# Kernel tuning notes

Hardware: AMD Instinct MI355X
Metric: run time of the kernel (lower is better)

## Reference

```python
import jax, jax.numpy as jnp
import numpy as np

DEPTH = 256
HEADS = 8
K = 128          # kernel_size == attended axis length (height)
DH = DEPTH // HEADS  # 32
EPS = 1e-5


def _bn(x, gamma, beta, axes):
    # training-mode batch norm (biased variance), per-channel on axis 1
    mean = jnp.mean(x, axis=axes, keepdims=True)
    var = jnp.var(x, axis=axes, keepdims=True)
    shape = [1] * x.ndim
    shape[1] = x.shape[1]
    g = gamma.reshape(shape)
    b = beta.reshape(shape)
    return (x - mean) * jax.lax.rsqrt(var + EPS) * g + b


def setup_inputs() -> dict:
    key = jax.random.key(0)
    ks = jax.random.split(key, 3)
    x = jax.random.normal(ks[0], (2, DEPTH, K, K), dtype=jnp.float32)
    w_kqv = jax.random.normal(ks[1], (2 * DEPTH, DEPTH), dtype=jnp.float32) * 0.05
    rel_encoding = jax.random.normal(ks[2], (2 * DH, 2 * K - 1), dtype=jnp.float32)
    return {
        "x": x,
        "w_kqv": w_kqv,
        "kqv_gamma": jnp.ones((2 * DEPTH,), jnp.float32),
        "kqv_beta": jnp.zeros((2 * DEPTH,), jnp.float32),
        "logits_gamma": jnp.ones((3 * HEADS,), jnp.float32),
        "logits_beta": jnp.zeros((3 * HEADS,), jnp.float32),
        "rel_encoding": rel_encoding,
    }


def reference(x, w_kqv, kqv_gamma, kqv_beta, logits_gamma, logits_beta, rel_encoding):
    B, C, H, W = x.shape  # height_dim=True path
    # (B,C,H,W) -> (B,W,C,H) -> (B*W, C, H)
    xf = jnp.transpose(x, (0, 3, 1, 2)).reshape(B * W, C, H)
    # 1x1 conv == channel matmul
    kqv = jnp.einsum('oc,bch->boh', w_kqv, xf)  # (BW, 2*depth, H)
    kqv = _bn(kqv, kqv_gamma, kqv_beta, axes=(0, 2))
    kqv = kqv.reshape(B * W, HEADS, 2 * DH, H)
    k = kqv[:, :, : DH // 2]            # (BW, h, dh/2, H)
    q = kqv[:, :, DH // 2: DH]          # (BW, h, dh/2, H)
    v = kqv[:, :, DH:]                  # (BW, h, dh,   H)

    # relative position gather: (2*dh, 2K-1) -> (2*dh, K, K)
    idx = (jnp.arange(K)[None, :] - jnp.arange(K)[:, None] + K - 1).reshape(-1)
    rel = rel_encoding[:, idx].reshape(2 * DH, K, K)
    q_enc = rel[: DH // 2]
    k_enc = rel[DH // 2: DH]
    v_enc = rel[DH:]

    qk = jnp.einsum('bhdx,bhdy->bhxy', q, k)
    qr = jnp.einsum('bhdx,dxy->bhxy', q, q_enc)
    kr = jnp.swapaxes(jnp.einsum('bhdx,dxy->bhxy', k, k_enc), 2, 3)
    logits = jnp.concatenate([qk, qr, kr], axis=1)  # (BW, 3*h, K, K)
    logits = _bn(logits, logits_gamma, logits_beta, axes=(0, 2, 3))
    logits = logits.reshape(B * W, 3, HEADS, H, H).sum(axis=1)
    weights = jax.nn.softmax(logits, axis=3)  # (BW, h, K, K)

    attn = jnp.einsum('bhxy,bhdy->bhdx', weights, v)         # (BW, h, dh, H)
    attn_enc = jnp.einsum('bhxy,dxy->bhdx', weights, v_enc)  # (BW, h, dh, H)
    out = (attn + attn_enc).reshape(B, W, DEPTH, H)  # cat+reshape+sum(dim=-2) == add
    out = jnp.transpose(out, (0, 2, 3, 1))  # (B, depth, H, W)
    return out
```

## Files before the change

kernel.cpp:

```cpp
#include <hip/hip_runtime.h>
#include <hip/hip_bf16.h>

#define H 128
#define NB 256
#define OC 512
#define CIN 256
#define NN 16384
#define EPS 1e-5f

typedef __attribute__((ext_vector_type(4))) float f32x4;
typedef __attribute__((ext_vector_type(8))) short bf16x8;
typedef unsigned short u16x8 __attribute__((ext_vector_type(8)));

__device__ __forceinline__ float bf2f(unsigned short u){
    return __uint_as_float(((unsigned int)u) << 16);
}
__device__ __forceinline__ unsigned short f2bf(float f){
    unsigned int x = __float_as_uint(f);
    return (unsigned short)((x + 0x7fffu + ((x >> 16) & 1u)) >> 16);
}
__device__ __forceinline__ float ldin(const void* p, size_t i, bool f32){
    return f32 ? ((const float*)p)[i] : bf2f(((const unsigned short*)p)[i]);
}
__device__ __forceinline__ short ld_bf16(const void* p, size_t i, bool f32){
    if (f32) return (short)f2bf(((const float*)p)[i]);
    return ((const short*)p)[i];
}
__device__ __forceinline__ bool probe_f32(const void* gamma_ones){
    return *(const unsigned int*)gamma_ones == 0x3F800000u;
}

template<bool F32>
__device__ __forceinline__ void gemm_body(const void* __restrict__ w,
                                          const void* __restrict__ x,
                                          unsigned short* __restrict__ c1,
                                          short (*As)[128][40], short (*Bs)[64][40])
{
    const int m0 = blockIdx.x * 128;
    const int n0 = blockIdx.y * 64;
    const int b0 = blockIdx.z;
    const int t  = threadIdx.x;
    const int lane = t & 63, wv = t >> 6;
    const int wm = wv & 1, wn = wv >> 1;
    const int lm = lane & 15, quad = lane >> 4;
    const size_t xb = (size_t)b0 * CIN * NN;
    const int am = t >> 1, ak = (t & 1) * 16;
    const int bn = t & 63, bk = (t >> 6) * 8;

    float4 pa[4]; float pb[8];
    u16x8 qa[2]; unsigned short qb[8];

    auto load_tile = [&](int k0){
        if constexpr (F32){
            const float* wp = (const float*)w + (size_t)(m0+am)*CIN + k0 + ak;
            #pragma unroll
            for (int q=0;q<4;q++) pa[q] = *(const float4*)(wp + 4*q);
            const float* xp = (const float*)x + xb + (size_t)(k0+bk)*NN + n0 + bn;
            #pragma unroll
            for (int i=0;i<8;i++) pb[i] = xp[(size_t)i*NN];
        } else {
            const unsigned short* wp = (const unsigned short*)w + (size_t)(m0+am)*CIN + k0 + ak;
            qa[0] = *(const u16x8*)wp; qa[1] = *(const u16x8*)(wp+8);
            const unsigned short* xp = (const unsigned short*)x + xb + (size_t)(k0+bk)*NN + n0 + bn;
            #pragma unroll
            for (int i=0;i<8;i++) qb[i] = xp[(size_t)i*NN];
        }
    };
    auto store_tile = [&](int buf){
        if constexpr (F32){
            short ta[16];
            #pragma unroll
            for (int q=0;q<4;q++){
                ta[4*q+0]=(short)f2bf(pa[q].x); ta[4*q+1]=(short)f2bf(pa[q].y);
                ta[4*q+2]=(short)f2bf(pa[q].z); ta[4*q+3]=(short)f2bf(pa[q].w);
            }
            *(bf16x8*)&As[buf][am][ak]   = *(bf16x8*)&ta[0];
            *(bf16x8*)&As[buf][am][ak+8] = *(bf16x8*)&ta[8];
            #pragma unroll
            for (int i=0;i<8;i++) Bs[buf][bn][bk+i] = (short)f2bf(pb[i]);
        } else {
            *(u16x8*)&As[buf][am][ak]   = qa[0];
            *(u16x8*)&As[buf][am][ak+8] = qa[1];
            #pragma unroll
            for (int i=0;i<8;i++) Bs[buf][bn][bk+i] = (short)qb[i];
        }
    };

    f32x4 acc[4][2];
    #pragma unroll
    for (int i=0;i<4;i++){ acc[i][0]=(f32x4){0,0,0,0}; acc[i][1]=(f32x4){0,0,0,0}; }

    load_tile(0); store_tile(0); __syncthreads();
    for (int kk=0; kk<8; ++kk){
        const int cur = kk & 1;
        if (kk < 7) load_tile((kk+1)*32);
        bf16x8 af[4], bfB[2];
        #pragma unroll
        for (int i=0;i<4;i++) af[i]  = *(const bf16x8*)&As[cur][wm*64 + i*16 + lm][quad*8];
        #pragma unroll
        for (int j=0;j<2;j++) bfB[j] = *(const bf16x8*)&Bs[cur][wn*32 + j*16 + lm][quad*8];
        #pragma unroll
        for (int i=0;i<4;i++)
            #pragma unroll
            for (int j=0;j<2;j++)
                acc[i][j] = __builtin_amdgcn_mfma_f32_16x16x32_bf16(af[i], bfB[j], acc[i][j], 0,0,0);
        if (kk < 7) store_tile(cur ^ 1);
        __syncthreads();
    }
    #pragma unroll
    for (int i=0;i<4;i++){
        #pragma unroll
        for (int j=0;j<2;j++){
            int n = n0 + wn*32 + j*16 + lm;
            #pragma unroll
            for (int r=0;r<4;r++){
                int m = m0 + wm*64 + i*16 + quad*4 + r;
                c1[((size_t)b0*OC + m)*NN + n] = f2bf(acc[i][j][r]);
            }
        }
    }
}

__global__ __launch_bounds__(256) void k_gemm(const void* __restrict__ w,
                                              const void* __restrict__ x,
                                              unsigned short* __restrict__ c1,
                                              const void* __restrict__ probe)
{
    __shared__ short As[2][128][40];
    __shared__ short Bs[2][64][40];
    if (probe_f32(probe)) gemm_body<true >(w, x, c1, As, Bs);
    else                  gemm_body<false>(w, x, c1, As, Bs);
}

__global__ __launch_bounds__(256) void k_bn_transpose(const unsigned short* __restrict__ c1,
        unsigned short* __restrict__ kqvt,
        const void* __restrict__ gamma, const void* __restrict__ beta)
{
    __shared__ float T[128][129];
    __shared__ float red[8];
    __shared__ float sc_sh[2];
    const bool f32 = probe_f32(gamma);
    const int o = blockIdx.x;
    const int t = threadIdx.x;
    const int lane = t & 63, wv = t >> 6;
    const unsigned short* r0 = c1 + (size_t)o*NN;
    const unsigned short* r1 = c1 + ((size_t)OC + o)*NN;
    const u16x8* r08 = (const u16x8*)r0;
    const u16x8* r18 = (const u16x8*)r1;
    float s=0.f, ss=0.f;
    #pragma unroll
    for (int i=0;i<8;i++){
        u16x8 a = r08[t + i*256];
        u16x8 b = r18[t + i*256];
        #pragma unroll
        for (int e=0;e<8;e++){
            float va = bf2f(a[e]); s += va; ss = fmaf(va,va,ss);
            float vb = bf2f(b[e]); s += vb; ss = fmaf(vb,vb,ss);
        }
    }
    #pragma unroll
    for (int off=1; off<64; off<<=1){ s += __shfl_xor(s,off); ss += __shfl_xor(ss,off); }
    if (lane==0){ red[wv*2] = s; red[wv*2+1] = ss; }
    __syncthreads();
    if (t==0){
        float st=0.f, sq=0.f;
        for (int i=0;i<4;i++){ st += red[i*2]; sq += red[i*2+1]; }
        float mean = st * (1.f/32768.f);
        float var  = sq * (1.f/32768.f) - mean*mean;
        float scale = ldin(gamma, o, f32) * rsqrtf(var + EPS);
        sc_sh[0] = scale;
        sc_sh[1] = ldin(beta, o, f32) - mean*scale;
    }
    __syncthreads();
    const float scale = sc_sh[0], shift = sc_sh[1];
    for (int b0=0;b0<2;b0++){
        const unsigned short* r = b0 ? r1 : r0;
        for (int i=0;i<64;i++){
            int idx = t + i*256;
            int h = idx >> 7, ww = idx & 127;
            T[ww][h] = fmaf(bf2f(r[idx]), scale, shift);
        }
        __syncthreads();
        for (int i=0;i<64;i++){
            int idx = t + i*256;
            int ww = idx >> 7, h = idx & 127;
            kqvt[(((size_t)(b0*128 + ww))*OC + o)*H + h] = f2bf(T[ww][h]);
        }
        __syncthreads();
    }
}

__global__ __launch_bounds__(256) void k_encpre(const void* __restrict__ relenc,
        float* __restrict__ ws, const void* __restrict__ probe)
{
    __shared__ float E[16][256];
    const bool f32 = probe_f32(probe);
    const int grp = blockIdx.x;
    const int t = threadIdx.x;
    for (int i = t; i < 16*255; i += 256){
        int d = i / 255, j = i - d*255;
        E[d][j] = bf2f((unsigned short)ld_bf16(relenc, (size_t)(grp*16 + d)*255 + j, f32));
    }
    __syncthreads();
    float* Rout = ws + 256  + grp*2048;
    float* Cout = ws + 8192 + grp*32768;
    {
        const int d = t >> 4, e = t & 15;
        const float* Ed = E[d]; const float* Ee = E[e];
        float c = 0.f;
        for (int j = 0; j < 128; ++j) c = fmaf(Ed[j], Ee[j], c);
        float* Cp = Cout + (d*16+e)*128;
        Cp[127] = c;
        for (int xx = 126; xx >= 0; --xx){
            c += Ed[254-xx]*Ee[254-xx] - Ed[126-xx]*Ee[126-xx];
            Cp[xx] = c;
        }
    }
    if (t < 16){
        const float* Ed = E[t];
        float r = 0.f;
        for (int j = 0; j < 128; ++j) r += Ed[j];
        float* Rp = Rout + t*128;
        Rp[127] = r;
        for (int xx = 126; xx >= 0; --xx){
            r += Ed[254-xx] - Ed[126-xx];
            Rp[xx] = r;
        }
    }
}

__global__ __launch_bounds__(256) void k_stats2(const unsigned short* __restrict__ kqvt,
        const float* __restrict__ ws, float* __restrict__ stats)
{
    __shared__ short QK[2][16][128];
    __shared__ float wr[4][6];
    const int b = blockIdx.x >> 3, head = blockIdx.x & 7;
    const int t = threadIdx.x;
    const int lane = t & 63, wv = t >> 6;
    const int lm = lane & 15, quad = lane >> 4;
    const unsigned short* base = kqvt + ((size_t)b*OC + head*64)*H;
    for (int i = t; i < 512; i += 256){
        int arr = i >> 8, d = (i >> 4) & 15, c = i & 15;
        *(u16x8*)&QK[arr][d][c*8] = *(const u16x8*)&base[(size_t)(arr*16 + d)*H + c*8];
    }
    __syncthreads();

    float s_qk = 0.f, q_qk = 0.f;
    if (wv == 0){
        f32x4 gq  = (f32x4){0,0,0,0}, gk  = (f32x4){0,0,0,0};
        f32x4 gq1 = (f32x4){0,0,0,0}, gk1 = (f32x4){0,0,0,0};
        bf16x8 ones;
        #pragma unroll
        for (int i=0;i<8;i++) ones[i] = (short)0x3F80;
        #pragma unroll
        for (int xt=0; xt<4; ++xt){
            bf16x8 fq = *(const bf16x8*)&QK[1][lm][xt*32 + quad*8];
            bf16x8 fk = *(const bf16x8*)&QK[0][lm][xt*32 + quad*8];
            gq  = __builtin_amdgcn_mfma_f32_16x16x32_bf16(fq, fq,   gq,  0,0,0);
            gk  = __builtin_amdgcn_mfma_f32_16x16x32_bf16(fk, fk,   gk,  0,0,0);
            gq1 = __builtin_amdgcn_mfma_f32_16x16x32_bf16(fq, ones, gq1, 0,0,0);
            gk1 = __builtin_amdgcn_mfma_f32_16x16x32_bf16(fk, ones, gk1, 0,0,0);
        }
        #pragma unroll
        for (int r=0;r<4;r++) q_qk += gq[r]*gk[r];
        if (lm == 0){
            #pragma unroll
            for (int r=0;r<4;r++) s_qk += gq1[r]*gk1[r];
        }
    }

    const int half = t >> 7;
    const int x = t & 127;
    float col[16];
    #pragma unroll
    for (int d=0; d<16; ++d) col[d] = bf2f((unsigned short)QK[1-half][d][x]);
    const float* Rp = ws + 256  + half*2048;
    const float* Cp = ws + 8192 + half*32768;
    float sr = 0.f, q2 = 0.f;
    #pragma unroll
    for (int d=0; d<16; ++d) sr = fmaf(col[d], Rp[d*128 + x], sr);
    for (int d=0; d<16; ++d){
        float qd = col[d];
        #pragma unroll
        for (int e=0; e<16; ++e)
            q2 = fmaf(qd*col[e], Cp[(d*16+e)*128 + x], q2);
    }
    float s_qr = half ? 0.f : sr,  q_qr = half ? 0.f : q2;
    float s_kr = half ? sr : 0.f,  q_kr = half ? q2 : 0.f;

    #pragma unroll
    for (int off=1; off<64; off<<=1){
        s_qk += __shfl_xor(s_qk,off); q_qk += __shfl_xor(q_qk,off);
        s_qr += __shfl_xor(s_qr,off); q_qr += __shfl_xor(q_qr,off);
        s_kr += __shfl_xor(s_kr,off); q_kr += __shfl_xor(q_kr,off);
    }
    if (lane==0){ wr[wv][0]=s_qk; wr[wv][1]=s_qr; wr[wv][2]=s_kr;
                  wr[wv][3]=q_qk; wr[wv][4]=q_qr; wr[wv][5]=q_kr; }
    __syncthreads();
    if (t==0){
        float a0=0,a1=0,a2=0,b0_=0,b1=0,b2=0;
        for (int i=0;i<4;i++){ a0+=wr[i][0]; a1+=wr[i][1]; a2+=wr[i][2];
                               b0_+=wr[i][3]; b1+=wr[i][4]; b2+=wr[i][5]; }
        atomicAdd(&stats[head],      a0);
        atomicAdd(&stats[8+head],    a1);
        atomicAdd(&stats[16+head],   a2);
        atomicAdd(&stats[24+head],   b0_);
        atomicAdd(&stats[32+head],   b1);
        atomicAdd(&stats[40+head],   b2);
    }
}

__global__ void k_scales(const float* __restrict__ stats, float* __restrict__ scales,
                         const void* __restrict__ gamma_l, const void* __restrict__ probe)
{
    const bool f32 = probe_f32(probe);
    int t = threadIdx.x;
    if (t < 24){
        const float inv_cnt = 1.f/4194304.f;
        float mean = stats[t]*inv_cnt;
        float var  = stats[24+t]*inv_cnt - mean*mean;
        scales[t] = ldin(gamma_l, t, f32) * rsqrtf(var + EPS);
    }
}

struct SA {
    short QA[128][40];
    short KA[128][40];
    short EQ[256][24];
    short EK[256][24];
};
struct SV {
    short Vs[32][136];
    short Evs[32][264];
};
union SU { SA a; SV v; };

__global__ __launch_bounds__(256) void k_attn(const unsigned short* __restrict__ kqvt,
        const void* __restrict__ relenc,
        const float* __restrict__ scales,
        void* __restrict__ outp,
        const void* __restrict__ probe)
{
    __shared__ SU smu;
    __shared__ short RW[128][136];
    __shared__ alignas(16) short ZED[16];
    const bool f32 = probe_f32(probe);
    const int blk = blockIdx.x;
    const int b = blk >> 3, head = blk & 7;
    const int b0 = b >> 7, w = b & 127;
    const int t = threadIdx.x;
    const int lane = t & 63, wv = t >> 6;
    const int lm = lane & 15, quad = lane >> 4;
    const unsigned short* base = kqvt + ((size_t)b*OC + head*64)*H;
    const float s0 = scales[head], s1 = scales[8+head], s2 = scales[16+head];

    {
        int dd = t & 15, xg = (t >> 4) * 8;
        u16x8 kv = *(const u16x8*)&base[dd*H + xg];
        u16x8 qv = *(const u16x8*)&base[(16+dd)*H + xg];
        #pragma unroll
        for (int e=0;e<8;e++){
            smu.a.QA[xg+e][dd] = (short)qv[e]; smu.a.QA[xg+e][16+dd] = 0;
            smu.a.KA[xg+e][dd] = (short)kv[e]; smu.a.KA[xg+e][16+dd] = 0;
        }
    }
    {
        int c = t & 15, jb = (t >> 4) * 16;
        short tq[16], tk[16];
        #pragma unroll
        for (int i=0;i<16;i++){
            int j = jb + i;
            float vq = (j<255) ? ldin(relenc, (size_t)c*255 + j, f32) : 0.f;
            float vk = (j<255) ? ldin(relenc, (size_t)(16+c)*255 + j, f32) : 0.f;
            tq[i] = (short)f2bf(s1*vq); tk[i] = (short)f2bf(s2*vk);
        }
        #pragma unroll
        for (int i=0;i<16;i++){ smu.a.EQ[jb+i][c] = tq[i]; smu.a.EK[jb+i][c] = tk[i]; }
    }
    if (t < 16) ZED[t] = 0;
    __syncthreads();

    f32x4 qacc[2][8];
    bf16x8 aq[2], akk[2];
    #pragma unroll
    for (int u=0;u<2;u++){
        const int mt = 2*wv + u;
        aq[u]  = *(const bf16x8*)&smu.a.QA[mt*16 + lm][quad*8];
        akk[u] = *(const bf16x8*)&smu.a.KA[mt*16 + lm][quad*8];
        #pragma unroll
        for (int yt=0; yt<8; ++yt){
            bf16x8 bk = *(const bf16x8*)&smu.a.KA[yt*16 + lm][quad*8];
            qacc[u][yt] = __builtin_amdgcn_mfma_f32_16x16x32_bf16(aq[u], bk,
                            (f32x4){0.f,0.f,0.f,0.f}, 0,0,0);
        }
        for (int jt=0; jt<16; ++jt){
            int sdiag = mt + jt;
            if (sdiag < 7 || sdiag > 15) continue;
            const short* pq = (quad < 2) ? &smu.a.EQ[jt*16 + lm][quad*8] : &ZED[0];
            f32x4 cq = __builtin_amdgcn_mfma_f32_16x16x32_bf16(aq[u], *(const bf16x8*)pq,
                         (f32x4){0.f,0.f,0.f,0.f}, 0,0,0);
            int j = jt*16 + lm;
            #pragma unroll
            for (int r=0;r<4;r++){
                int x = mt*16 + quad*4 + r;
                int y = x + j - 127;
                if ((unsigned)y < 128u) RW[x][y] = (short)f2bf(cq[r]);
            }
        }
    }
    __syncthreads();

    #pragma unroll
    for (int u=0;u<2;u++){
        const int mt = 2*wv + u;
        for (int jt=0; jt<16; ++jt){
            int sdiag = mt + jt;
            if (sdiag < 7 || sdiag > 15) continue;
            const short* pk = (quad < 2) ? &smu.a.EK[jt*16 + lm][quad*8] : &ZED[0];
            f32x4 ck = __builtin_amdgcn_mfma_f32_16x16x32_bf16(akk[u], *(const bf16x8*)pk,
                         (f32x4){0.f,0.f,0.f,0.f}, 0,0,0);
            int j = jt*16 + lm;
            #pragma unroll
            for (int r=0;r<4;r++){
                int y = mt*16 + quad*4 + r;
                int x = y + j - 127;
                if ((unsigned)x < 128u){
                    float cur = bf2f((unsigned short)RW[x][y]);
                    RW[x][y] = (short)f2bf(cur + ck[r]);
                }
            }
        }
    }
    __syncthreads();

    {
        int dd = t & 31, yg = (t >> 5) * 16;
        u16x8 v0 = *(const u16x8*)&base[(32+dd)*H + yg];
        u16x8 v1 = *(const u16x8*)&base[(32+dd)*H + yg + 8];
        *(u16x8*)&smu.v.Vs[dd][yg]   = v0;
        *(u16x8*)&smu.v.Vs[dd][yg+8] = v1;
    }
    {
        int d = t & 31, jb = (t >> 5) * 32;
        short tv[32];
        #pragma unroll
        for (int i=0;i<32;i++){
            int j = jb + i;
            tv[i] = (j < 255) ? ld_bf16(relenc, (size_t)(32+d)*255 + j, f32) : (short)0;
        }
        #pragma unroll
        for (int i=0;i<32;i+=8)
            *(u16x8*)&smu.v.Evs[d][jb+i] = *(u16x8*)&tv[i];
        if ((t >> 5) == 7)
            *(u16x8*)&smu.v.Evs[d][256] = (u16x8){0,0,0,0,0,0,0,0};
    }
    #pragma unroll
    for (int u=0;u<2;u++){
        const int mt = 2*wv + u;
        #pragma unroll
        for (int r=0;r<4;r++){
            const int x = mt*16 + quad*4 + r;
            float v[8]; float mx = -1e30f;
            #pragma unroll
            for (int yt=0; yt<8; ++yt){
                v[yt] = fmaf(s0, qacc[u][yt][r], bf2f((unsigned short)RW[x][yt*16 + lm]));
                mx = fmaxf(mx, v[yt]);
            }
            mx = fmaxf(mx, __shfl_xor(mx,1));
            mx = fmaxf(mx, __shfl_xor(mx,2));
            mx = fmaxf(mx, __shfl_xor(mx,4));
            mx = fmaxf(mx, __shfl_xor(mx,8));
            float sum = 0.f;
            #pragma unroll
            for (int yt=0; yt<8; ++yt){ v[yt] = __expf(v[yt]-mx); sum += v[yt]; }
            sum += __shfl_xor(sum,1);
            sum += __shfl_xor(sum,2);
            sum += __shfl_xor(sum,4);
            sum += __shfl_xor(sum,8);
            float inv = 1.f/sum;
            #pragma unroll
            for (int yt=0; yt<8; ++yt)
                RW[x][yt*16 + lm] = (short)f2bf(v[yt]*inv);
        }
    }
    __syncthreads();

    f32x4 o[2][2];
    #pragma unroll
    for (int u=0;u<2;u++){ o[u][0]=(f32x4){0,0,0,0}; o[u][1]=(f32x4){0,0,0,0}; }
    #pragma unroll
    for (int kt=0; kt<4; ++kt){
        bf16x8 bv0 = *(const bf16x8*)&smu.v.Vs[lm][kt*32 + quad*8];
        bf16x8 bv1 = *(const bf16x8*)&smu.v.Vs[16+lm][kt*32 + quad*8];
        #pragma unroll
        for (int u=0;u<2;u++){
            bf16x8 aw = *(const bf16x8*)&RW[(2*wv+u)*16 + lm][kt*32 + quad*8];
            o[u][0] = __builtin_amdgcn_mfma_f32_16x16x32_bf16(aw, bv0, o[u][0], 0,0,0);
            o[u][1] = __builtin_amdgcn_mfma_f32_16x16x32_bf16(aw, bv1, o[u][1], 0,0,0);
        }
    }
    for (int kt=0; kt<8; ++kt){
        bf16x8 be0 = *(const bf16x8*)&smu.v.Evs[lm][kt*32 + quad*8];
        bf16x8 be1 = *(const bf16x8*)&smu.v.Evs[16+lm][kt*32 + quad*8];
        #pragma unroll
        for (int u=0;u<2;u++){
            const int mt = 2*wv + u;
            int lo = mt*16 + kt*32 - 127;
            if (lo > 127 || lo + 46 < 0) continue;
            int xg = mt*16 + lm;
            int y0 = xg + kt*32 + quad*8 - 127;
            short g[8];
            #pragma unroll
            for (int jj=0;jj<8;jj++){
                int y = y0 + jj;
                g[jj] = ((unsigned)y < 128u) ? RW[xg][y] : (short)0;
            }
            bf16x8 ag = *(bf16x8*)g;
            o[u][0] = __builtin_amdgcn_mfma_f32_16x16x32_bf16(ag, be0, o[u][0], 0,0,0);
            o[u][1] = __builtin_amdgcn_mfma_f32_16x16x32_bf16(ag, be1, o[u][1], 0,0,0);
        }
    }
    #pragma unroll
    for (int u=0;u<2;u++){
        #pragma unroll
        for (int nt=0; nt<2; ++nt){
            int d = nt*16 + lm;
            size_t cb = ((size_t)(b0*256 + head*32 + d))*16384 + (size_t)w;
            #pragma unroll
            for (int r=0;r<4;r++){
                int x = (2*wv+u)*16 + quad*4 + r;
                if (f32) ((float*)outp)[cb + (size_t)x*128] = o[u][nt][r];
                else ((unsigned short*)outp)[cb + (size_t)x*128] = f2bf(o[u][nt][r]);
            }
        }
    }
}

extern "C" void kernel_launch(void* const* d_in, const int* in_sizes, int n_in,
                              void* d_out, int out_size, void* d_ws, size_t ws_size,
                              hipStream_t stream)
{
    (void)in_sizes; (void)n_in; (void)out_size;
    const void* x      = d_in[0];
    const void* w_kqv  = d_in[1];
    const void* kqv_g  = d_in[2];
    const void* kqv_b  = d_in[3];
    const void* log_g  = d_in[4];
    const void* relenc = d_in[6];

    if (ws_size < (size_t)64*1024*1024) return;
    unsigned short* C1   = (unsigned short*)d_ws;
    unsigned short* KQVT = C1 + 16777216;
    float* WS     = (float*)d_ws;
    float* STATS  = WS;
    float* SCALES = WS + 48;

    dim3 g1(OC/128, NN/64, 2);
    k_gemm<<<g1, 256, 0, stream>>>(w_kqv, x, C1, kqv_g);
    k_bn_transpose<<<512, 256, 0, stream>>>(C1, KQVT, kqv_g, kqv_b);
    hipMemsetAsync(STATS, 0, 48*sizeof(float), stream);
    k_encpre<<<2, 256, 0, stream>>>(relenc, WS, kqv_g);
    k_stats2<<<2048, 256, 0, stream>>>(KQVT, WS, STATS);
    k_scales<<<1, 64, 0, stream>>>(STATS, SCALES, log_g, kqv_g);
    k_attn<<<2048, 256, 0, stream>>>(KQVT, relenc, SCALES, d_out, kqv_g);
}
```

Measured before the change: 397.8 us.

## Precompute scaled relative-encoding tables once and read them from global in attention

Adds a small kernel that builds per-head scaled bf16 Q/K encoding tables, and extends the encoding-prep kernel to build a padded V encoding table, all in workspace. The attention kernel now reads these tables directly from global/L2 instead of having each of its 2048 blocks reload, convert and scale the encodings into shared memory. This shrinks shared memory (QA/KA padding cut, EQ/EK/Evs removed), which may allow more resident blocks, and the V tile load moves earlier. The cost is uncoalesced-ish global loads inside the MFMA loops and one extra launch; the workspace offsets must not overlap C1/KQVT or stats.

Result: faster. 369.1 us (-7.2%).

```diff
diff --git a/kernel.cpp b/kernel.cpp
--- a/kernel.cpp
+++ b/kernel.cpp
@@ -7,6 +7,10 @@
 #define CIN 256
 #define NN 16384
 #define EPS 1e-5f
+
+#define EQG_OFF 524288
+#define EKG_OFF 589824
+#define EVG_OFF 655360
 
 typedef __attribute__((ext_vector_type(4))) float f32x4;
 typedef __attribute__((ext_vector_type(8))) short bf16x8;
@@ -197,6 +201,14 @@
     const bool f32 = probe_f32(probe);
     const int grp = blockIdx.x;
     const int t = threadIdx.x;
+    if (grp == 2){
+        unsigned short* ev = (unsigned short*)ws + EVG_OFF;
+        for (int i = t; i < 32*264; i += 256){
+            int d = i / 264, j = i - d*264;
+            ev[i] = (j < 255) ? (unsigned short)ld_bf16(relenc, (size_t)(32+d)*255 + j, f32) : 0;
+        }
+        return;
+    }
     for (int i = t; i < 16*255; i += 256){
         int d = i / 255, j = i - d*255;
         E[d][j] = bf2f((unsigned short)ld_bf16(relenc, (size_t)(grp*16 + d)*255 + j, f32));
@@ -323,20 +335,37 @@
     }
 }
 
+__global__ void k_escale(const void* __restrict__ relenc, const float* __restrict__ scales,
+                         unsigned short* __restrict__ etab, const void* __restrict__ probe)
+{
+    const bool f32 = probe_f32(probe);
+    const int head = blockIdx.x;
+    const int t = threadIdx.x;
+    const float s1 = scales[8+head], s2 = scales[16+head];
+    unsigned short* eq = etab + EQG_OFF + head*8192;
+    unsigned short* ek = etab + EKG_OFF + head*8192;
+    for (int i = t; i < 8192; i += 256){
+        int j = i >> 5, c = i & 31;
+        unsigned short vq = 0, vk = 0;
+        if (c < 16 && j < 255){
+            vq = f2bf(s1 * ldin(relenc, (size_t)c*255 + j, f32));
+            vk = f2bf(s2 * ldin(relenc, (size_t)(16+c)*255 + j, f32));
+        }
+        eq[i] = vq; ek[i] = vk;
+    }
+}
+
 struct SA {
-    short QA[128][40];
-    short KA[128][40];
-    short EQ[256][24];
-    short EK[256][24];
+    short QA[128][24];
+    short KA[128][24];
 };
 struct SV {
     short Vs[32][136];
-    short Evs[32][264];
 };
 union SU { SA a; SV v; };
 
 __global__ __launch_bounds__(256) void k_attn(const unsigned short* __restrict__ kqvt,
-        const void* __restrict__ relenc,
+        const unsigned short* __restrict__ etab,
         const float* __restrict__ scales,
         void* __restrict__ outp,
         const void* __restrict__ probe)
@@ -352,7 +381,10 @@
     const int lane = t & 63, wv = t >> 6;
     const int lm = lane & 15, quad = lane >> 4;
     const unsigned short* base = kqvt + ((size_t)b*OC + head*64)*H;
-    const float s0 = scales[head], s1 = scales[8+head], s2 = scales[16+head];
+    const float s0 = scales[head];
+    const unsigned short* EQg = etab + EQG_OFF + (size_t)head*8192;
+    const unsigned short* EKg = etab + EKG_OFF + (size_t)head*8192;
+    const unsigned short* EVg = etab + EVG_OFF;
 
     {
         int dd = t & 15, xg = (t >> 4) * 8;
@@ -360,22 +392,9 @@
         u16x8 qv = *(const u16x8*)&base[(16+dd)*H + xg];
         #pragma unroll
         for (int e=0;e<8;e++){
-            smu.a.QA[xg+e][dd] = (short)qv[e]; smu.a.QA[xg+e][16+dd] = 0;
-            smu.a.KA[xg+e][dd] = (short)kv[e]; smu.a.KA[xg+e][16+dd] = 0;
-        }
-    }
-    {
-        int c = t & 15, jb = (t >> 4) * 16;
-        short tq[16], tk[16];
-        #pragma unroll
-        for (int i=0;i<16;i++){
-            int j = jb + i;
-            float vq = (j<255) ? ldin(relenc, (size_t)c*255 + j, f32) : 0.f;
-            float vk = (j<255) ? ldin(relenc, (size_t)(16+c)*255 + j, f32) : 0.f;
-            tq[i] = (short)f2bf(s1*vq); tk[i] = (short)f2bf(s2*vk);
-        }
-        #pragma unroll
-        for (int i=0;i<16;i++){ smu.a.EQ[jb+i][c] = tq[i]; smu.a.EK[jb+i][c] = tk[i]; }
+            smu.a.QA[xg+e][dd] = (short)qv[e];
+            smu.a.KA[xg+e][dd] = (short)kv[e];
+        }
     }
     if (t < 16) ZED[t] = 0;
     __syncthreads();
@@ -385,19 +404,22 @@
     #pragma unroll
     for (int u=0;u<2;u++){
         const int mt = 2*wv + u;
-        aq[u]  = *(const bf16x8*)&smu.a.QA[mt*16 + lm][quad*8];
-        akk[u] = *(const bf16x8*)&smu.a.KA[mt*16 + lm][quad*8];
+        const short* pa  = (quad < 2) ? &smu.a.QA[mt*16 + lm][quad*8] : &ZED[0];
+        const short* pk0 = (quad < 2) ? &smu.a.KA[mt*16 + lm][quad*8] : &ZED[0];
+        aq[u]  = *(const bf16x8*)pa;
+        akk[u] = *(const bf16x8*)pk0;
         #pragma unroll
         for (int yt=0; yt<8; ++yt){
-            bf16x8 bk = *(const bf16x8*)&smu.a.KA[yt*16 + lm][quad*8];
+            const short* pb = (quad < 2) ? &smu.a.KA[yt*16 + lm][quad*8] : &ZED[0];
+            bf16x8 bk = *(const bf16x8*)pb;
             qacc[u][yt] = __builtin_amdgcn_mfma_f32_16x16x32_bf16(aq[u], bk,
                             (f32x4){0.f,0.f,0.f,0.f}, 0,0,0);
         }
         for (int jt=0; jt<16; ++jt){
             int sdiag = mt + jt;
             if (sdiag < 7 || sdiag > 15) continue;
-            const short* pq = (quad < 2) ? &smu.a.EQ[jt*16 + lm][quad*8] : &ZED[0];
-            f32x4 cq = __builtin_amdgcn_mfma_f32_16x16x32_bf16(aq[u], *(const bf16x8*)pq,
+            bf16x8 bq = *(const bf16x8*)&EQg[(size_t)(jt*16 + lm)*32 + quad*8];
+            f32x4 cq = __builtin_amdgcn_mfma_f32_16x16x32_bf16(aq[u], bq,
                          (f32x4){0.f,0.f,0.f,0.f}, 0,0,0);
             int j = jt*16 + lm;
             #pragma unroll
@@ -410,14 +432,21 @@
     }
     __syncthreads();
 
+    {
+        int dd = t & 31, yg = (t >> 5) * 16;
+        u16x8 v0 = *(const u16x8*)&base[(32+dd)*H + yg];
+        u16x8 v1 = *(const u16x8*)&base[(32+dd)*H + yg + 8];
+        *(u16x8*)&smu.v.Vs[dd][yg]   = v0;
+        *(u16x8*)&smu.v.Vs[dd][yg+8] = v1;
+    }
     #pragma unroll
     for (int u=0;u<2;u++){
         const int mt = 2*wv + u;
         for (int jt=0; jt<16; ++jt){
             int sdiag = mt + jt;
             if (sdiag < 7 || sdiag > 15) continue;
-            const short* pk = (quad < 2) ? &smu.a.EK[jt*16 + lm][quad*8] : &ZED[0];
-            f32x4 ck = __builtin_amdgcn_mfma_f32_16x16x32_bf16(akk[u], *(const bf16x8*)pk,
+            bf16x8 bkE = *(const bf16x8*)&EKg[(size_t)(jt*16 + lm)*32 + quad*8];
+            f32x4 ck = __builtin_amdgcn_mfma_f32_16x16x32_bf16(akk[u], bkE,
                          (f32x4){0.f,0.f,0.f,0.f}, 0,0,0);
             int j = jt*16 + lm;
             #pragma unroll
@@ -433,27 +462,6 @@
     }
     __syncthreads();
 
-    {
-        int dd = t & 31, yg = (t >> 5) * 16;
-        u16x8 v0 = *(const u16x8*)&base[(32+dd)*H + yg];
-        u16x8 v1 = *(const u16x8*)&base[(32+dd)*H + yg + 8];
-        *(u16x8*)&smu.v.Vs[dd][yg]   = v0;
-        *(u16x8*)&smu.v.Vs[dd][yg+8] = v1;
-    }
-    {
-        int d = t & 31, jb = (t >> 5) * 32;
-        short tv[32];
-        #pragma unroll
-        for (int i=0;i<32;i++){
-            int j = jb + i;
-            tv[i] = (j < 255) ? ld_bf16(relenc, (size_t)(32+d)*255 + j, f32) : (short)0;
-        }
-        #pragma unroll
-        for (int i=0;i<32;i+=8)
-            *(u16x8*)&smu.v.Evs[d][jb+i] = *(u16x8*)&tv[i];
-        if ((t >> 5) == 7)
-            *(u16x8*)&smu.v.Evs[d][256] = (u16x8){0,0,0,0,0,0,0,0};
-    }
     #pragma unroll
     for (int u=0;u<2;u++){
         const int mt = 2*wv + u;
@@ -500,8 +508,8 @@
         }
     }
     for (int kt=0; kt<8; ++kt){
-        bf16x8 be0 = *(const bf16x8*)&smu.v.Evs[lm][kt*32 + quad*8];
-        bf16x8 be1 = *(const bf16x8*)&smu.v.Evs[16+lm][kt*32 + quad*8];
+        bf16x8 be0 = *(const bf16x8*)&EVg[(size_t)lm*264      + kt*32 + quad*8];
+        bf16x8 be1 = *(const bf16x8*)&EVg[(size_t)(16+lm)*264 + kt*32 + quad*8];
         #pragma unroll
         for (int u=0;u<2;u++){
             const int mt = 2*wv + u;
@@ -554,13 +562,15 @@
     float* WS     = (float*)d_ws;
     float* STATS  = WS;
     float* SCALES = WS + 48;
+    unsigned short* ETAB = (unsigned short*)d_ws;
 
     dim3 g1(OC/128, NN/64, 2);
     k_gemm<<<g1, 256, 0, stream>>>(w_kqv, x, C1, kqv_g);
     k_bn_transpose<<<512, 256, 0, stream>>>(C1, KQVT, kqv_g, kqv_b);
     hipMemsetAsync(STATS, 0, 48*sizeof(float), stream);
-    k_encpre<<<2, 256, 0, stream>>>(relenc, WS, kqv_g);
+    k_encpre<<<3, 256, 0, stream>>>(relenc, WS, kqv_g);
     k_stats2<<<2048, 256, 0, stream>>>(KQVT, WS, STATS);
     k_scales<<<1, 64, 0, stream>>>(STATS, SCALES, log_g, kqv_g);
-    k_attn<<<2048, 256, 0, stream>>>(KQVT, relenc, SCALES, d_out, kqv_g);
-}
+    k_escale<<<8, 256, 0, stream>>>(relenc, SCALES, ETAB, kqv_g);
+    k_attn<<<2048, 256, 0, stream>>>(KQVT, ETAB, SCALES, d_out, kqv_g);
+}
```
